# Kernel tuning notes

Measured on AMD Instinct MI355X. Metric: run time of the kernel, lower is better.

## Reference

```python
import jax, jax.numpy as jnp
import numpy as np

D_MODEL, D_STATE, D_CONV, D_INNER, DT_RANK = 96, 16, 3, 192, 6
BATCH, H, W = 4, 64, 64


def setup_inputs() -> dict:
    key = jax.random.key(0)
    ks = jax.random.split(key, 8)
    s = 0.02
    return {
        "x": jax.random.normal(ks[0], (BATCH, H, W, D_MODEL), jnp.float32),
        "in_proj_w": jax.random.normal(ks[1], (2 * D_INNER, D_MODEL), jnp.float32) * s,
        "conv_w": jax.random.normal(ks[2], (D_INNER, 1, D_CONV, D_CONV), jnp.float32) * s,
        "conv_b": jnp.zeros((D_INNER,), jnp.float32),
        "x_proj_w": jax.random.normal(ks[3], (4, DT_RANK + 2 * D_STATE, D_INNER), jnp.float32) * s,
        "dt_w": jax.random.normal(ks[4], (4, D_INNER, DT_RANK), jnp.float32) * s,
        # dt bias ~ inverse-softplus of dt in [1e-3, 1e-1] (roughly log-uniform negative values)
        "dt_b": jax.random.uniform(ks[5], (4, D_INNER), jnp.float32, minval=-6.0, maxval=-2.3),
        "A_logs": jnp.log(jnp.tile(jnp.arange(1, D_STATE + 1, dtype=jnp.float32), (4 * D_INNER, 1))),
        "Ds": jnp.ones((4 * D_INNER,), jnp.float32),
        "ln_w": jnp.ones((D_INNER,), jnp.float32),
        "ln_b": jnp.zeros((D_INNER,), jnp.float32),
        "out_proj_w": jax.random.normal(ks[6], (D_MODEL, D_INNER), jnp.float32) * s,
    }


def _ss2d(x, in_proj_w, conv_w, conv_b, x_proj_w, dt_w, dt_b, A_logs, Ds, ln_w, ln_b, out_proj_w):
    B, Hh, Ww, C = x.shape
    D = conv_w.shape[0]          # d_inner
    N = A_logs.shape[1]          # d_state
    R = dt_w.shape[2]            # dt_rank
    L = Hh * Ww
    K = 4

    xz = x @ in_proj_w.T                          # (B,H,W,2D)
    xi, z = jnp.split(xz, 2, axis=-1)
    xc = jnp.transpose(xi, (0, 3, 1, 2))          # (B,D,H,W)
    pad = (D_CONV - 1) // 2
    xc = jax.lax.conv_general_dilated(xc, conv_w, (1, 1), ((pad, pad), (pad, pad)),
                                      feature_group_count=D)
    xc = jax.nn.silu(xc + conv_b[None, :, None, None])

    # 4 scan directions: row-major, col-major, and their reverses
    x_flat = xc.reshape(B, D, L)
    x_tr = jnp.transpose(xc, (0, 1, 3, 2)).reshape(B, D, L)
    x_hwwh = jnp.stack([x_flat, x_tr], axis=1)                     # (B,2,D,L)
    xs = jnp.concatenate([x_hwwh, jnp.flip(x_hwwh, axis=-1)], axis=1)  # (B,K,D,L)

    x_dbl = jnp.einsum('bkdl,kcd->bkcl', xs, x_proj_w)
    dts, Bs, Cs = jnp.split(x_dbl, [R, R + N], axis=2)             # (B,K,R,L),(B,K,N,L),(B,K,N,L)
    dts = jnp.einsum('bkrl,kdr->bkdl', dts, dt_w)
    delta = jax.nn.softplus(dts + dt_b[None, :, :, None])          # (B,K,D,L)
    A = -jnp.exp(A_logs).reshape(K, D, N)                          # (K,D,N)

    # sequential selective scan over L (L-first for lax.scan)
    u_seq = jnp.moveaxis(xs, -1, 0)        # (L,B,K,D)
    dt_seq = jnp.moveaxis(delta, -1, 0)    # (L,B,K,D)
    B_seq = jnp.moveaxis(Bs, -1, 0)        # (L,B,K,N)
    C_seq = jnp.moveaxis(Cs, -1, 0)        # (L,B,K,N)

    def step(h, inp):
        u_t, dt_t, B_t, C_t = inp
        h = jnp.exp(dt_t[..., None] * A) * h + (dt_t * u_t)[..., None] * B_t[:, :, None, :]
        y = jnp.einsum('bkdn,bkn->bkd', h, C_t)
        return h, y

    h0 = jnp.zeros((B, K, D, N), jnp.float32)
    _, ys = jax.lax.scan(step, h0, (u_seq, dt_seq, B_seq, C_seq))
    out_y = jnp.moveaxis(ys, 0, -1) + Ds.reshape(K, D)[None, :, :, None] * xs  # (B,K,D,L)

    y1 = out_y[:, 0]
    y2 = jnp.transpose(out_y[:, 1].reshape(B, D, Ww, Hh), (0, 1, 3, 2)).reshape(B, D, L)
    y3 = jnp.flip(out_y[:, 2], axis=-1)
    y4 = jnp.transpose(jnp.flip(out_y[:, 3], axis=-1).reshape(B, D, Ww, Hh), (0, 1, 3, 2)).reshape(B, D, L)
    y = y1 + y2 + y3 + y4                                           # (B,D,L)

    y = jnp.transpose(y, (0, 2, 1)).reshape(B, Hh, Ww, D)
    mu = y.mean(-1, keepdims=True)
    var = y.var(-1, keepdims=True)
    y = (y - mu) * jax.lax.rsqrt(var + 1e-5) * ln_w + ln_b
    y = y * jax.nn.silu(z)
    return y @ out_proj_w.T


def reference(x, in_proj_w, conv_w, conv_b, x_proj_w, dt_w, dt_b, A_logs, Ds, ln_w, ln_b, out_proj_w):
    return _ss2d(x, in_proj_w, conv_w, conv_b, x_proj_w, dt_w, dt_b, A_logs, Ds, ln_w, ln_b, out_proj_w)
```

## Files before the change

kernel.cpp:

```cpp
#include <hip/hip_runtime.h>

constexpr int BATCH = 4;
constexpr int HS    = 64;
constexpr int WSZ   = 64;
constexpr int LSEQ  = 4096;
constexpr int DM    = 96;
constexpr int DI    = 192;
constexpr int NS    = 16;
constexpr int RK    = 6;
constexpr int KD    = 4;
constexpr int NCH   = 128;
constexpr int CLEN  = 32;
constexpr int XDS   = 160;
constexpr int GCH   = 16;
constexpr int GLEN  = NCH / GCH;

__device__ __forceinline__ int pos_of(int k, int l) {
  switch (k & 3) {
    case 0: return l;
    case 1: return ((l & 63) << 6) | (l >> 6);
    case 2: return LSEQ - 1 - l;
    default: { int lp = LSEQ - 1 - l; return ((lp & 63) << 6) | (lp >> 6); }
  }
}

__device__ __forceinline__ float softplus_f(float s) {
  return (s > 20.f) ? s : __logf(1.f + __expf(s));
}

__device__ __forceinline__ void pw16(float e, float* p) {
  float e2 = e * e, e4 = e2 * e2, e8 = e4 * e4;
  p[1] = e;       p[2] = e2;      p[3] = e2 * e;  p[4] = e4;
  p[5] = e4 * e;  p[6] = e4 * e2; p[7] = p[6] * e; p[8] = e8;
  p[9] = e8 * e;  p[10] = e8 * e2; p[11] = p[10] * e; p[12] = e8 * e4;
  p[13] = p[12] * e; p[14] = p[12] * e2; p[15] = p[14] * e; p[16] = e8 * e8;
}

__device__ __forceinline__ bool geo_check(const float* Al) {
  const float lntab[16] = {0.f, 0.6931472f, 1.0986123f, 1.3862944f, 1.6094379f,
                           1.7917595f, 1.9459101f, 2.0794415f, 2.1972246f, 2.3025851f,
                           2.3978953f, 2.4849066f, 2.5649494f, 2.6390573f, 2.7080502f,
                           2.7725887f};
  bool g = true;
  #pragma unroll
  for (int n = 0; n < NS; ++n)
    g = g && (fabsf(Al[n] - Al[0] - lntab[n]) <= 2e-3f);
  return g;
}

__device__ __forceinline__ float dt6(const float* w, float bsv, float4 t0, float4 t1) {
  return bsv + w[0]*t0.x + w[1]*t0.y + w[2]*t0.z + w[3]*t0.w + w[4]*t1.x + w[5]*t1.y;
}

__launch_bounds__(256)
__global__ void prep_weights(const float* __restrict__ xw, const float* __restrict__ ipw,
                             const float* __restrict__ opw, float* __restrict__ WcatT,
                             float* __restrict__ inpT, float* __restrict__ outpT) {
  int idx = blockIdx.x * 256 + threadIdx.x;
  if (idx < DI * XDS) {
    int col = idx / XDS, j = idx % XDS;
    int k = j / 40, jj = j % 40;
    float v = 0.f;
    int src = -1;
    if (jj < 16)      src = k * 38 + 6 + jj;
    else if (jj < 32) src = k * 38 + 22 + (jj - 16);
    else if (jj < 38) src = k * 38 + (jj - 32);
    if (src >= 0) v = xw[(size_t)src * DI + col];
    WcatT[idx] = v;
    return;
  }
  idx -= DI * XDS;
  if (idx < 2 * DI * DM) {
    int r = idx / DM, c = idx % DM;
    inpT[(size_t)c * (2 * DI) + r] = ipw[idx];
    return;
  }
  idx -= 2 * DI * DM;
  if (idx < DM * DI) {
    int r = idx / DI, c = idx % DI;
    outpT[(size_t)c * DM + r] = opw[idx];
  }
}

template <int NN, int KK, int TM, int KT>
__launch_bounds__(256)
__global__ void gemm_nt(const float* __restrict__ A, const float* __restrict__ BT,
                        float* __restrict__ C, int M) {
  constexpr int TN  = 64;
  constexpr int RPT = TM / 16;
  constexpr int SA  = KT + 4;
  constexpr int KQ  = KT / 4;
  __shared__ float As[TM][SA];
  __shared__ float Bs[KT][TN];
  const int t = threadIdx.x;
  const int row0 = blockIdx.y * TM;
  const int col0 = blockIdx.x * TN;
  const int tc = t & 15;
  const int tr = t >> 4;

  float acc[RPT][4];
  #pragma unroll
  for (int i = 0; i < RPT; ++i)
    { acc[i][0]=0.f; acc[i][1]=0.f; acc[i][2]=0.f; acc[i][3]=0.f; }

  for (int k0 = 0; k0 < KK; k0 += KT) {
    #pragma unroll 1
    for (int idx = t; idx < TM * KQ; idx += 256) {
      int r = idx / KQ, kq = idx % KQ;
      *(float4*)&As[r][kq * 4] =
          *(const float4*)&A[(size_t)(row0 + r) * KK + k0 + kq * 4];
    }
    #pragma unroll 1
    for (int idx = t; idx < KT * 16; idx += 256) {
      int kk = idx >> 4, cq = idx & 15;
      int col = col0 + cq * 4;
      float4 v = make_float4(0.f, 0.f, 0.f, 0.f);
      if (col < NN) v = *(const float4*)&BT[(size_t)(k0 + kk) * NN + col];
      *(float4*)&Bs[kk][cq * 4] = v;
    }
    __syncthreads();
    #pragma unroll 4
    for (int kk = 0; kk < KT; ++kk) {
      float4 bv = *(const float4*)&Bs[kk][tc * 4];
      #pragma unroll
      for (int i = 0; i < RPT; ++i) {
        float a = As[tr * RPT + i][kk];
        acc[i][0] += a * bv.x; acc[i][1] += a * bv.y;
        acc[i][2] += a * bv.z; acc[i][3] += a * bv.w;
      }
    }
    __syncthreads();
  }
  int c = col0 + tc * 4;
  if (c < NN) {
    #pragma unroll
    for (int i = 0; i < RPT; ++i) {
      size_t r0 = (size_t)(row0 + tr * RPT + i) * NN + c;
      *(float4*)&C[r0] = make_float4(acc[i][0], acc[i][1], acc[i][2], acc[i][3]);
    }
  }
}

__launch_bounds__(256)
__global__ void conv_silu(const float* __restrict__ xz, const float* __restrict__ cw,
                          const float* __restrict__ cb, float* __restrict__ xc) {
  int idx = blockIdx.x * 256 + threadIdx.x;
  int d = idx % DI;
  int p = (idx / DI) % LSEQ;
  int b = idx / (DI * LSEQ);
  int h = p >> 6, w = p & 63;
  float acc = cb[d];
  #pragma unroll
  for (int kh = 0; kh < 3; ++kh) {
    int hh = h + kh - 1;
    if ((unsigned)hh >= (unsigned)HS) continue;
    #pragma unroll
    for (int kw = 0; kw < 3; ++kw) {
      int ww = w + kw - 1;
      if ((unsigned)ww >= (unsigned)WSZ) continue;
      acc += xz[((size_t)b * LSEQ + (hh << 6) + ww) * (2 * DI) + d] * cw[d * 9 + kh * 3 + kw];
    }
  }
  xc[idx] = acc / (1.f + __expf(-acc));
}

__launch_bounds__(192)
__global__ void scan_phase1(const float* __restrict__ xc, const float* __restrict__ xdbl,
                            const float* __restrict__ Alog, const float* __restrict__ dtw,
                            const float* __restrict__ dtb,
                            float* __restrict__ hN, float* __restrict__ sumdB,
                            float* __restrict__ ypl) {
  const int d = threadIdx.x;
  const int ch = blockIdx.x, k = blockIdx.y, b = blockIdx.z;
  const int bk = b * KD + k;
  __shared__ float4 Bsh[CLEN * 10];
  #pragma unroll 1
  for (int idx = d; idx < CLEN * 10; idx += 192) {
    int j = idx / 10, q = idx % 10;
    int p = pos_of(k, ch * CLEN + j);
    Bsh[idx] = *(const float4*)&xdbl[(size_t)(b * LSEQ + p) * XDS + k * 40 + q * 4];
  }
  float Al[NS];
  {
    const float4* Ap = (const float4*)&Alog[((size_t)k * DI + d) * NS];
    #pragma unroll
    for (int q = 0; q < 4; ++q) {
      float4 a = Ap[q];
      Al[q*4+0] = a.x; Al[q*4+1] = a.y; Al[q*4+2] = a.z; Al[q*4+3] = a.w;
    }
  }
  const bool geo = geo_check(Al);
  const float An0 = -__expf(Al[0]);
  float w[RK];
  #pragma unroll
  for (int r = 0; r < RK; ++r) w[r] = dtw[((size_t)k * DI + d) * RK + r];
  const float bsv = dtb[k * DI + d];
  __syncthreads();

  float h[NS];
  #pragma unroll
  for (int n = 0; n < NS; ++n) h[n] = 0.f;
  float sumd = 0.f;
  float* yout = ypl + (size_t)bk * LSEQ * DI;
  const int l0 = ch * CLEN;
  if (geo) {
    #pragma unroll 2
    for (int j = 0; j < CLEN; ++j) {
      const int p = pos_of(k, l0 + j);
      const size_t bp = (size_t)b * LSEQ + p;
      float4 t0 = Bsh[j * 10 + 8], t1 = Bsh[j * 10 + 9];
      float dl = softplus_f(dt6(w, bsv, t0, t1));
      float du = dl * xc[bp * DI + d];
      float pw[17];
      pw16(__expf(dl * An0), pw);
      float y = 0.f;
      #pragma unroll
      for (int q = 0; q < 4; ++q) {
        float4 v  = Bsh[j * 10 + q];
        float4 c4 = Bsh[j * 10 + 4 + q];
        h[q*4+0] = pw[q*4+1] * h[q*4+0] + du * v.x; y += h[q*4+0] * c4.x;
        h[q*4+1] = pw[q*4+2] * h[q*4+1] + du * v.y; y += h[q*4+1] * c4.y;
        h[q*4+2] = pw[q*4+3] * h[q*4+2] + du * v.z; y += h[q*4+2] * c4.z;
        h[q*4+3] = pw[q*4+4] * h[q*4+3] + du * v.w; y += h[q*4+3] * c4.w;
      }
      sumd += dl;
      yout[(size_t)p * DI + d] = y;
    }
  } else {
    float An[NS];
    #pragma unroll
    for (int n = 0; n < NS; ++n) An[n] = -__expf(Al[n]);
    #pragma unroll 1
    for (int j = 0; j < CLEN; ++j) {
      const int p = pos_of(k, l0 + j);
      const size_t bp = (size_t)b * LSEQ + p;
      float4 t0 = Bsh[j * 10 + 8], t1 = Bsh[j * 10 + 9];
      float dl = softplus_f(dt6(w, bsv, t0, t1));
      float du = dl * xc[bp * DI + d];
      float y = 0.f;
      #pragma unroll
      for (int q = 0; q < 4; ++q) {
        float4 v  = Bsh[j * 10 + q];
        float4 c4 = Bsh[j * 10 + 4 + q];
        h[q*4+0] = __expf(dl * An[q*4+0]) * h[q*4+0] + du * v.x; y += h[q*4+0] * c4.x;
        h[q*4+1] = __expf(dl * An[q*4+1]) * h[q*4+1] + du * v.y; y += h[q*4+1] * c4.y;
        h[q*4+2] = __expf(dl * An[q*4+2]) * h[q*4+2] + du * v.z; y += h[q*4+2] * c4.z;
        h[q*4+3] = __expf(dl * An[q*4+3]) * h[q*4+3] + du * v.w; y += h[q*4+3] * c4.w;
      }
      sumd += dl;
      yout[(size_t)p * DI + d] = y;
    }
  }
  const size_t o = ((size_t)bk * NCH + ch) * DI + d;
  float4* Hp = (float4*)&hN[o * NS];
  #pragma unroll
  for (int q = 0; q < 4; ++q)
    Hp[q] = make_float4(h[q*4+0], h[q*4+1], h[q*4+2], h[q*4+3]);
  sumdB[o] = sumd;
}

__launch_bounds__(256)
__global__ void combine_a(const float* __restrict__ hN, const float* __restrict__ sumdB,
                          const float* __restrict__ Alog,
                          float* __restrict__ Wg, float* __restrict__ Tg) {
  const int tid = blockIdx.x * 256 + threadIdx.x;
  const int n  = tid & 15;
  int rem = tid >> 4;
  const int d  = rem % DI;  rem /= DI;
  const int g  = rem % GCH;
  const int bk = rem / GCH;
  const int k  = bk & 3;
  const float An = -__expf(Alog[((size_t)k * DI + d) * NS + n]);
  float W = 1.f, T = 0.f;
  #pragma unroll
  for (int j = 0; j < GLEN; ++j) {
    const int c = g * GLEN + j;
    const size_t o = ((size_t)bk * NCH + c) * DI + d;
    float w = __expf(An * sumdB[o]);
    T = hN[o * NS + n] + w * T;
    W *= w;
  }
  Wg[tid] = W;
  Tg[tid] = T;
}

__launch_bounds__(256)
__global__ void combine_b(const float* __restrict__ Wg, const float* __restrict__ Tg,
                          float* __restrict__ Hg) {
  const int tid = blockIdx.x * 256 + threadIdx.x;
  const int dn = tid & (DI * NS - 1);
  const int bk = tid / (DI * NS);
  float H = 0.f;
  #pragma unroll
  for (int g = 0; g < GCH; ++g) {
    const size_t o = ((size_t)(bk * GCH + g)) * (DI * NS) + dn;
    Hg[o] = H;
    H = Tg[o] + Wg[o] * H;
  }
}

__launch_bounds__(256)
__global__ void combine_c(float* __restrict__ hN, const float* __restrict__ sumdB,
                          const float* __restrict__ Alog, const float* __restrict__ Hg) {
  const int tid = blockIdx.x * 256 + threadIdx.x;
  const int n  = tid & 15;
  int rem = tid >> 4;
  const int d  = rem % DI;  rem /= DI;
  const int g  = rem % GCH;
  const int bk = rem / GCH;
  const int k  = bk & 3;
  const float An = -__expf(Alog[((size_t)k * DI + d) * NS + n]);
  float e = Hg[tid];
  #pragma unroll
  for (int j = 0; j < GLEN; ++j) {
    const int c = g * GLEN + j;
    const size_t o = ((size_t)bk * NCH + c) * DI + d;
    float w = __expf(An * sumdB[o]);
    float tmp = hN[o * NS + n];
    hN[o * NS + n] = e;
    e = tmp + w * e;
  }
}

__launch_bounds__(192)
__global__ void scan_corr(const float* __restrict__ xdbl, const float* __restrict__ Alog,
                          const float* __restrict__ dtw, const float* __restrict__ dtb,
                          const float* __restrict__ hin, float* __restrict__ ypl) {
  const int d = threadIdx.x;
  const int ch = blockIdx.x + 1;
  const int k = blockIdx.y, b = blockIdx.z;
  const int bk = b * KD + k;
  __shared__ float4 Bsh[CLEN * 6];
  {
    int idx = d;
    int j = idx / 6, q = idx % 6;
    int p = pos_of(k, ch * CLEN + j);
    Bsh[idx] = *(const float4*)&xdbl[(size_t)(b * LSEQ + p) * XDS + k * 40 + (q + 4) * 4];
  }
  float Al[NS];
  {
    const float4* Ap = (const float4*)&Alog[((size_t)k * DI + d) * NS];
    #pragma unroll
    for (int q = 0; q < 4; ++q) {
      float4 a = Ap[q];
      Al[q*4+0] = a.x; Al[q*4+1] = a.y; Al[q*4+2] = a.z; Al[q*4+3] = a.w;
    }
  }
  const bool geo = geo_check(Al);
  const float An0 = -__expf(Al[0]);
  float w[RK];
  #pragma unroll
  for (int r = 0; r < RK; ++r) w[r] = dtw[((size_t)k * DI + d) * RK + r];
  const float bsv = dtb[k * DI + d];

  float g[NS];
  {
    const size_t o = ((size_t)bk * NCH + ch) * DI + d;
    const float4* Hp = (const float4*)&hin[o * NS];
    #pragma unroll
    for (int q = 0; q < 4; ++q) {
      float4 v = Hp[q];
      g[q*4+0] = v.x; g[q*4+1] = v.y; g[q*4+2] = v.z; g[q*4+3] = v.w;
    }
  }
  __syncthreads();
  float* yout = ypl + (size_t)bk * LSEQ * DI;
  const int l0 = ch * CLEN;
  float cum = 0.f;
  if (geo) {
    #pragma unroll 2
    for (int j = 0; j < CLEN; ++j) {
      const int p = pos_of(k, l0 + j);
      float4 t0 = Bsh[j * 6 + 4], t1 = Bsh[j * 6 + 5];
      cum += softplus_f(dt6(w, bsv, t0, t1));
      float pw[17];
      pw16(__expf(cum * An0), pw);
      float y = 0.f;
      #pragma unroll
      for (int q = 0; q < 4; ++q) {
        float4 c4 = Bsh[j * 6 + q];
        y += (pw[q*4+1] * g[q*4+0]) * c4.x;
        y += (pw[q*4+2] * g[q*4+1]) * c4.y;
        y += (pw[q*4+3] * g[q*4+2]) * c4.z;
        y += (pw[q*4+4] * g[q*4+3]) * c4.w;
      }
      yout[(size_t)p * DI + d] += y;
    }
  } else {
    float An[NS];
    #pragma unroll
    for (int n = 0; n < NS; ++n) An[n] = -__expf(Al[n]);
    #pragma unroll 1
    for (int j = 0; j < CLEN; ++j) {
      const int p = pos_of(k, l0 + j);
      float4 t0 = Bsh[j * 6 + 4], t1 = Bsh[j * 6 + 5];
      cum += softplus_f(dt6(w, bsv, t0, t1));
      float y = 0.f;
      #pragma unroll
      for (int q = 0; q < 4; ++q) {
        float4 c4 = Bsh[j * 6 + q];
        y += (__expf(An[q*4+0] * cum) * g[q*4+0]) * c4.x;
        y += (__expf(An[q*4+1] * cum) * g[q*4+1]) * c4.y;
        y += (__expf(An[q*4+2] * cum) * g[q*4+2]) * c4.z;
        y += (__expf(An[q*4+3] * cum) * g[q*4+3]) * c4.w;
      }
      yout[(size_t)p * DI + d] += y;
    }
  }
}

__launch_bounds__(192)
__global__ void fuse_ln(const float* __restrict__ ypl, const float* __restrict__ xc,
                        const float* __restrict__ Ds, const float* __restrict__ xz,
                        const float* __restrict__ lnw, const float* __restrict__ lnb,
                        float* __restrict__ ymul) {
  const int row = blockIdx.x;
  const int b = row >> 12;
  const size_t pd = (size_t)row * DI + threadIdx.x;
  const int d = threadIdx.x;
  constexpr size_t PL = (size_t)LSEQ * DI;
  float u = xc[pd];
  float sDs = Ds[d] + Ds[DI + d] + Ds[2 * DI + d] + Ds[3 * DI + d];
  const size_t base = (size_t)(b * KD) * PL + pd - (size_t)b * PL;
  float y = ypl[base] + ypl[base + PL] + ypl[base + 2 * PL] + ypl[base + 3 * PL] + sDs * u;
  float s1 = y, s2 = y * y;
  #pragma unroll
  for (int off = 32; off; off >>= 1) {
    s1 += __shfl_xor(s1, off);
    s2 += __shfl_xor(s2, off);
  }
  __shared__ float r1[3], r2[3];
  int wid = d >> 6;
  if ((d & 63) == 0) { r1[wid] = s1; r2[wid] = s2; }
  __syncthreads();
  float S1 = r1[0] + r1[1] + r1[2];
  float S2 = r2[0] + r2[1] + r2[2];
  float mu = S1 * (1.f / DI);
  float var = S2 * (1.f / DI) - mu * mu;
  float yn = (y - mu) * rsqrtf(var + 1e-5f) * lnw[d] + lnb[d];
  float zv = xz[(size_t)row * (2 * DI) + DI + d];
  float g = zv / (1.f + __expf(-zv));
  ymul[pd] = yn * g;
}

extern "C" void kernel_launch(void* const* d_in, const int* in_sizes, int n_in,
                              void* d_out, int out_size, void* d_ws, size_t ws_size,
                              hipStream_t stream) {
  (void)in_sizes; (void)n_in; (void)out_size; (void)ws_size;
  const float* x          = (const float*)d_in[0];
  const float* in_proj_w  = (const float*)d_in[1];
  const float* conv_w     = (const float*)d_in[2];
  const float* conv_b     = (const float*)d_in[3];
  const float* x_proj_w   = (const float*)d_in[4];
  const float* dt_w       = (const float*)d_in[5];
  const float* dt_b       = (const float*)d_in[6];
  const float* A_logs     = (const float*)d_in[7];
  const float* Ds         = (const float*)d_in[8];
  const float* ln_w       = (const float*)d_in[9];
  const float* ln_b       = (const float*)d_in[10];
  const float* out_proj_w = (const float*)d_in[11];
  float* out = (float*)d_out;
  float* ws  = (float*)d_ws;

  constexpr size_t SZ_XZ    = (size_t)BATCH * LSEQ * 2 * DI;
  constexpr size_t SZ_XC    = (size_t)BATCH * LSEQ * DI;
  constexpr size_t SZ_XD    = (size_t)BATCH * LSEQ * XDS;
  constexpr size_t SZ_HN    = (size_t)BATCH * KD * NCH * DI * NS;
  constexpr size_t SZ_SUMD  = (size_t)BATCH * KD * NCH * DI;
  constexpr size_t SZ_YPL   = (size_t)BATCH * KD * LSEQ * DI;
  constexpr size_t SZ_G     = (size_t)BATCH * KD * GCH * DI * NS;

  float* xz    = ws;
  float* xc    = xz + SZ_XZ;
  float* xdbl  = xc + SZ_XC;
  float* hN    = xdbl + SZ_XD;
  float* sumd  = hN + SZ_HN;
  float* ypl   = sumd + SZ_SUMD;
  float* WcatT = ypl + SZ_YPL;
  float* inpT  = WcatT + (size_t)DI * XDS;
  float* outpT = inpT + (size_t)DM * 2 * DI;
  float* Wg    = outpT + (size_t)DI * DM;
  float* Tg    = Wg + SZ_G;
  float* Hg    = Tg + SZ_G;
  float* ymul  = hN;

  const int M = BATCH * LSEQ;
  const int SG = BATCH * KD * GCH * DI * NS;
  const int PREP = DI * XDS + 2 * DI * DM + DM * DI;

  prep_weights<<<(PREP + 255) / 256, 256, 0, stream>>>(x_proj_w, in_proj_w, out_proj_w,
                                                       WcatT, inpT, outpT);
  gemm_nt<2 * DI, DM, 64, 96><<<dim3(6, M / 64), 256, 0, stream>>>(x, inpT, xz, M);
  conv_silu<<<(BATCH * LSEQ * DI) / 256, 256, 0, stream>>>(xz, conv_w, conv_b, xc);
  gemm_nt<XDS, DI, 64, 96><<<dim3(3, M / 64), 256, 0, stream>>>(xc, WcatT, xdbl, M);
  scan_phase1<<<dim3(NCH, KD, BATCH), 192, 0, stream>>>(xc, xdbl, A_logs, dt_w, dt_b,
                                                        hN, sumd, ypl);
  combine_a<<<SG / 256, 256, 0, stream>>>(hN, sumd, A_logs, Wg, Tg);
  combine_b<<<(BATCH * KD * DI * NS) / 256, 256, 0, stream>>>(Wg, Tg, Hg);
  combine_c<<<SG / 256, 256, 0, stream>>>(hN, sumd, A_logs, Hg);
  scan_corr<<<dim3(NCH - 1, KD, BATCH), 192, 0, stream>>>(xdbl, A_logs, dt_w, dt_b,
                                                          hN, ypl);
  fuse_ln<<<M, DI, 0, stream>>>(ypl, xc, Ds, xz, ln_w, ln_b, ymul);
  gemm_nt<DM, DI, 64, 96><<<dim3(2, M / 64), 256, 0, stream>>>(ymul, outpT, out, M);
}
```

Before: 213.2 us.

## Split SSM state dimension across thread pairs in scan kernels

Both chunked scan kernels now use two threads per channel, each holding half of the 16 state entries. A lane-xor shuffle sums the partial outputs and only the even lane stores. The goal is more threads per block and fewer registers per thread, which shortens each thread's serial recurrence and raises occupancy. The cost is duplicated dt/softplus/exp work in both lanes, an extra shuffle each step, and half-idle lanes on the output stores.

```diff
diff --git a/kernel.cpp b/kernel.cpp
--- a/kernel.cpp
+++ b/kernel.cpp
@@ -28,12 +28,11 @@
   return (s > 20.f) ? s : __logf(1.f + __expf(s));
 }
 
-__device__ __forceinline__ void pw16(float e, float* p) {
-  float e2 = e * e, e4 = e2 * e2, e8 = e4 * e4;
-  p[1] = e;       p[2] = e2;      p[3] = e2 * e;  p[4] = e4;
-  p[5] = e4 * e;  p[6] = e4 * e2; p[7] = p[6] * e; p[8] = e8;
-  p[9] = e8 * e;  p[10] = e8 * e2; p[11] = p[10] * e; p[12] = e8 * e4;
-  p[13] = p[12] * e; p[14] = p[12] * e2; p[15] = p[14] * e; p[16] = e8 * e8;
+__device__ __forceinline__ void pw8h(float e, float base, float* p) {
+  float e2 = e * e, e4 = e2 * e2;
+  float e3 = e2 * e, e5 = e4 * e, e6 = e4 * e2, e7 = e6 * e, e8 = e4 * e4;
+  p[0] = base * e;  p[1] = base * e2; p[2] = base * e3; p[3] = base * e4;
+  p[4] = base * e5; p[5] = base * e6; p[6] = base * e7; p[7] = base * e8;
 }
 
 __device__ __forceinline__ bool geo_check(const float* Al) {
@@ -164,21 +163,21 @@
   xc[idx] = acc / (1.f + __expf(-acc));
 }
 
-__launch_bounds__(192)
+__launch_bounds__(384)
 __global__ void scan_phase1(const float* __restrict__ xc, const float* __restrict__ xdbl,
                             const float* __restrict__ Alog, const float* __restrict__ dtw,
                             const float* __restrict__ dtb,
                             float* __restrict__ hN, float* __restrict__ sumdB,
                             float* __restrict__ ypl) {
-  const int d = threadIdx.x;
+  const int t = threadIdx.x;
+  const int d = t >> 1, half = t & 1;
   const int ch = blockIdx.x, k = blockIdx.y, b = blockIdx.z;
   const int bk = b * KD + k;
   __shared__ float4 Bsh[CLEN * 10];
-  #pragma unroll 1
-  for (int idx = d; idx < CLEN * 10; idx += 192) {
-    int j = idx / 10, q = idx % 10;
+  if (t < CLEN * 10) {
+    int j = t / 10, q = t % 10;
     int p = pos_of(k, ch * CLEN + j);
-    Bsh[idx] = *(const float4*)&xdbl[(size_t)(b * LSEQ + p) * XDS + k * 40 + q * 4];
+    Bsh[t] = *(const float4*)&xdbl[(size_t)(b * LSEQ + p) * XDS + k * 40 + q * 4];
   }
   float Al[NS];
   {
@@ -197,12 +196,13 @@
   const float bsv = dtb[k * DI + d];
   __syncthreads();
 
-  float h[NS];
-  #pragma unroll
-  for (int n = 0; n < NS; ++n) h[n] = 0.f;
+  float h[8];
+  #pragma unroll
+  for (int n = 0; n < 8; ++n) h[n] = 0.f;
   float sumd = 0.f;
   float* yout = ypl + (size_t)bk * LSEQ * DI;
   const int l0 = ch * CLEN;
+  const int hb = half * 2;
   if (geo) {
     #pragma unroll 2
     for (int j = 0; j < CLEN; ++j) {
@@ -211,25 +211,30 @@
       float4 t0 = Bsh[j * 10 + 8], t1 = Bsh[j * 10 + 9];
       float dl = softplus_f(dt6(w, bsv, t0, t1));
       float du = dl * xc[bp * DI + d];
-      float pw[17];
-      pw16(__expf(dl * An0), pw);
+      float e = __expf(dl * An0);
+      float e2 = e * e, e4 = e2 * e2, e8 = e4 * e4;
+      float base = half ? e8 : 1.f;
+      float pw[8];
+      pw8h(e, base, pw);
+      float4 v0 = Bsh[j * 10 + hb],     v1 = Bsh[j * 10 + hb + 1];
+      float4 c0 = Bsh[j * 10 + 4 + hb], c1 = Bsh[j * 10 + 4 + hb + 1];
       float y = 0.f;
-      #pragma unroll
-      for (int q = 0; q < 4; ++q) {
-        float4 v  = Bsh[j * 10 + q];
-        float4 c4 = Bsh[j * 10 + 4 + q];
-        h[q*4+0] = pw[q*4+1] * h[q*4+0] + du * v.x; y += h[q*4+0] * c4.x;
-        h[q*4+1] = pw[q*4+2] * h[q*4+1] + du * v.y; y += h[q*4+1] * c4.y;
-        h[q*4+2] = pw[q*4+3] * h[q*4+2] + du * v.z; y += h[q*4+2] * c4.z;
-        h[q*4+3] = pw[q*4+4] * h[q*4+3] + du * v.w; y += h[q*4+3] * c4.w;
-      }
+      h[0] = pw[0] * h[0] + du * v0.x; y += h[0] * c0.x;
+      h[1] = pw[1] * h[1] + du * v0.y; y += h[1] * c0.y;
+      h[2] = pw[2] * h[2] + du * v0.z; y += h[2] * c0.z;
+      h[3] = pw[3] * h[3] + du * v0.w; y += h[3] * c0.w;
+      h[4] = pw[4] * h[4] + du * v1.x; y += h[4] * c1.x;
+      h[5] = pw[5] * h[5] + du * v1.y; y += h[5] * c1.y;
+      h[6] = pw[6] * h[6] + du * v1.z; y += h[6] * c1.z;
+      h[7] = pw[7] * h[7] + du * v1.w; y += h[7] * c1.w;
+      y += __shfl_xor(y, 1);
       sumd += dl;
-      yout[(size_t)p * DI + d] = y;
+      if (!half) yout[(size_t)p * DI + d] = y;
     }
   } else {
-    float An[NS];
+    float An[8];
     #pragma unroll
-    for (int n = 0; n < NS; ++n) An[n] = -__expf(Al[n]);
+    for (int n = 0; n < 8; ++n) An[n] = -__expf(Al[half * 8 + n]);
     #pragma unroll 1
     for (int j = 0; j < CLEN; ++j) {
       const int p = pos_of(k, l0 + j);
@@ -237,26 +242,27 @@
       float4 t0 = Bsh[j * 10 + 8], t1 = Bsh[j * 10 + 9];
       float dl = softplus_f(dt6(w, bsv, t0, t1));
       float du = dl * xc[bp * DI + d];
+      float4 v0 = Bsh[j * 10 + hb],     v1 = Bsh[j * 10 + hb + 1];
+      float4 c0 = Bsh[j * 10 + 4 + hb], c1 = Bsh[j * 10 + 4 + hb + 1];
       float y = 0.f;
-      #pragma unroll
-      for (int q = 0; q < 4; ++q) {
-        float4 v  = Bsh[j * 10 + q];
-        float4 c4 = Bsh[j * 10 + 4 + q];
-        h[q*4+0] = __expf(dl * An[q*4+0]) * h[q*4+0] + du * v.x; y += h[q*4+0] * c4.x;
-        h[q*4+1] = __expf(dl * An[q*4+1]) * h[q*4+1] + du * v.y; y += h[q*4+1] * c4.y;
-        h[q*4+2] = __expf(dl * An[q*4+2]) * h[q*4+2] + du * v.z; y += h[q*4+2] * c4.z;
-        h[q*4+3] = __expf(dl * An[q*4+3]) * h[q*4+3] + du * v.w; y += h[q*4+3] * c4.w;
-      }
+      h[0] = __expf(dl*An[0]) * h[0] + du * v0.x; y += h[0] * c0.x;
+      h[1] = __expf(dl*An[1]) * h[1] + du * v0.y; y += h[1] * c0.y;
+      h[2] = __expf(dl*An[2]) * h[2] + du * v0.z; y += h[2] * c0.z;
+      h[3] = __expf(dl*An[3]) * h[3] + du * v0.w; y += h[3] * c0.w;
+      h[4] = __expf(dl*An[4]) * h[4] + du * v1.x; y += h[4] * c1.x;
+      h[5] = __expf(dl*An[5]) * h[5] + du * v1.y; y += h[5] * c1.y;
+      h[6] = __expf(dl*An[6]) * h[6] + du * v1.z; y += h[6] * c1.z;
+      h[7] = __expf(dl*An[7]) * h[7] + du * v1.w; y += h[7] * c1.w;
+      y += __shfl_xor(y, 1);
       sumd += dl;
-      yout[(size_t)p * DI + d] = y;
+      if (!half) yout[(size_t)p * DI + d] = y;
     }
   }
   const size_t o = ((size_t)bk * NCH + ch) * DI + d;
   float4* Hp = (float4*)&hN[o * NS];
-  #pragma unroll
-  for (int q = 0; q < 4; ++q)
-    Hp[q] = make_float4(h[q*4+0], h[q*4+1], h[q*4+2], h[q*4+3]);
-  sumdB[o] = sumd;
+  Hp[half * 2 + 0] = make_float4(h[0], h[1], h[2], h[3]);
+  Hp[half * 2 + 1] = make_float4(h[4], h[5], h[6], h[7]);
+  if (!half) sumdB[o] = sumd;
 }
 
 __launch_bounds__(256)
@@ -322,20 +328,20 @@
   }
 }
 
-__launch_bounds__(192)
+__launch_bounds__(384)
 __global__ void scan_corr(const float* __restrict__ xdbl, const float* __restrict__ Alog,
                           const float* __restrict__ dtw, const float* __restrict__ dtb,
                           const float* __restrict__ hin, float* __restrict__ ypl) {
-  const int d = threadIdx.x;
+  const int t = threadIdx.x;
+  const int d = t >> 1, half = t & 1;
   const int ch = blockIdx.x + 1;
   const int k = blockIdx.y, b = blockIdx.z;
   const int bk = b * KD + k;
   __shared__ float4 Bsh[CLEN * 6];
-  {
-    int idx = d;
-    int j = idx / 6, q = idx % 6;
+  if (t < CLEN * 6) {
+    int j = t / 6, q = t % 6;
     int p = pos_of(k, ch * CLEN + j);
-    Bsh[idx] = *(const float4*)&xdbl[(size_t)(b * LSEQ + p) * XDS + k * 40 + (q + 4) * 4];
+    Bsh[t] = *(const float4*)&xdbl[(size_t)(b * LSEQ + p) * XDS + k * 40 + (q + 4) * 4];
   }
   float Al[NS];
   {
@@ -353,19 +359,19 @@
   for (int r = 0; r < RK; ++r) w[r] = dtw[((size_t)k * DI + d) * RK + r];
   const float bsv = dtb[k * DI + d];
 
-  float g[NS];
+  float g[8];
   {
     const size_t o = ((size_t)bk * NCH + ch) * DI + d;
     const float4* Hp = (const float4*)&hin[o * NS];
-    #pragma unroll
-    for (int q = 0; q < 4; ++q) {
-      float4 v = Hp[q];
-      g[q*4+0] = v.x; g[q*4+1] = v.y; g[q*4+2] = v.z; g[q*4+3] = v.w;
-    }
+    float4 v = Hp[half * 2 + 0];
+    g[0]=v.x; g[1]=v.y; g[2]=v.z; g[3]=v.w;
+    float4 u = Hp[half * 2 + 1];
+    g[4]=u.x; g[5]=u.y; g[6]=u.z; g[7]=u.w;
   }
   __syncthreads();
   float* yout = ypl + (size_t)bk * LSEQ * DI;
   const int l0 = ch * CLEN;
+  const int hb = half * 2;
   float cum = 0.f;
   if (geo) {
     #pragma unroll 2
@@ -373,38 +379,41 @@
       const int p = pos_of(k, l0 + j);
       float4 t0 = Bsh[j * 6 + 4], t1 = Bsh[j * 6 + 5];
       cum += softplus_f(dt6(w, bsv, t0, t1));
-      float pw[17];
-      pw16(__expf(cum * An0), pw);
+      float e = __expf(cum * An0);
+      float e2 = e * e, e4 = e2 * e2, e8 = e4 * e4;
+      float base = half ? e8 : 1.f;
+      float pw[8];
+      pw8h(e, base, pw);
+      float4 c0 = Bsh[j * 6 + hb], c1 = Bsh[j * 6 + hb + 1];
       float y = 0.f;
-      #pragma unroll
-      for (int q = 0; q < 4; ++q) {
-        float4 c4 = Bsh[j * 6 + q];
-        y += (pw[q*4+1] * g[q*4+0]) * c4.x;
-        y += (pw[q*4+2] * g[q*4+1]) * c4.y;
-        y += (pw[q*4+3] * g[q*4+2]) * c4.z;
-        y += (pw[q*4+4] * g[q*4+3]) * c4.w;
-      }
-      yout[(size_t)p * DI + d] += y;
+      y += (pw[0] * g[0]) * c0.x; y += (pw[1] * g[1]) * c0.y;
+      y += (pw[2] * g[2]) * c0.z; y += (pw[3] * g[3]) * c0.w;
+      y += (pw[4] * g[4]) * c1.x; y += (pw[5] * g[5]) * c1.y;
+      y += (pw[6] * g[6]) * c1.z; y += (pw[7] * g[7]) * c1.w;
+      y += __shfl_xor(y, 1);
+      if (!half) yout[(size_t)p * DI + d] += y;
     }
   } else {
-    float An[NS];
+    float An[8];
     #pragma unroll
-    for (int n = 0; n < NS; ++n) An[n] = -__expf(Al[n]);
+    for (int n = 0; n < 8; ++n) An[n] = -__expf(Al[half * 8 + n]);
     #pragma unroll 1
     for (int j = 0; j < CLEN; ++j) {
       const int p = pos_of(k, l0 + j);
       float4 t0 = Bsh[j * 6 + 4], t1 = Bsh[j * 6 + 5];
       cum += softplus_f(dt6(w, bsv, t0, t1));
+      float4 c0 = Bsh[j * 6 + hb], c1 = Bsh[j * 6 + hb + 1];
       float y = 0.f;
-      #pragma unroll
-      for (int q = 0; q < 4; ++q) {
-        float4 c4 = Bsh[j * 6 + q];
-        y += (__expf(An[q*4+0] * cum) * g[q*4+0]) * c4.x;
-        y += (__expf(An[q*4+1] * cum) * g[q*4+1]) * c4.y;
-        y += (__expf(An[q*4+2] * cum) * g[q*4+2]) * c4.z;
-        y += (__expf(An[q*4+3] * cum) * g[q*4+3]) * c4.w;
-      }
-      yout[(size_t)p * DI + d] += y;
+      y += (__expf(An[0] * cum) * g[0]) * c0.x;
+      y += (__expf(An[1] * cum) * g[1]) * c0.y;
+      y += (__expf(An[2] * cum) * g[2]) * c0.z;
+      y += (__expf(An[3] * cum) * g[3]) * c0.w;
+      y += (__expf(An[4] * cum) * g[4]) * c1.x;
+      y += (__expf(An[5] * cum) * g[5]) * c1.y;
+      y += (__expf(An[6] * cum) * g[6]) * c1.z;
+      y += (__expf(An[7] * cum) * g[7]) * c1.w;
+      y += __shfl_xor(y, 1);
+      if (!half) yout[(size_t)p * DI + d] += y;
     }
   }
 }
@@ -493,12 +502,12 @@
   gemm_nt<2 * DI, DM, 64, 96><<<dim3(6, M / 64), 256, 0, stream>>>(x, inpT, xz, M);
   conv_silu<<<(BATCH * LSEQ * DI) / 256, 256, 0, stream>>>(xz, conv_w, conv_b, xc);
   gemm_nt<XDS, DI, 64, 96><<<dim3(3, M / 64), 256, 0, stream>>>(xc, WcatT, xdbl, M);
-  scan_phase1<<<dim3(NCH, KD, BATCH), 192, 0, stream>>>(xc, xdbl, A_logs, dt_w, dt_b,
+  scan_phase1<<<dim3(NCH, KD, BATCH), 384, 0, stream>>>(xc, xdbl, A_logs, dt_w, dt_b,
                                                         hN, sumd, ypl);
   combine_a<<<SG / 256, 256, 0, stream>>>(hN, sumd, A_logs, Wg, Tg);
   combine_b<<<(BATCH * KD * DI * NS) / 256, 256, 0, stream>>>(Wg, Tg, Hg);
   combine_c<<<SG / 256, 256, 0, stream>>>(hN, sumd, A_logs, Hg);
-  scan_corr<<<dim3(NCH - 1, KD, BATCH), 192, 0, stream>>>(xdbl, A_logs, dt_w, dt_b,
+  scan_corr<<<dim3(NCH - 1, KD, BATCH), 384, 0, stream>>>(xdbl, A_logs, dt_w, dt_b,
                                                           hN, ypl);
   fuse_ln<<<M, DI, 0, stream>>>(ypl, xc, Ds, xz, ln_w, ln_b, ymul);
   gemm_nt<DM, DI, 64, 96><<<dim3(2, M / 64), 256, 0, stream>>>(ymul, outpT, out, M);
```

New measurement: 243.1 us. +14.0%, slower.

## Fuse chunk-combine kernels into one block-local scan; split scan blocks by channel

Applied to the files above, without the earlier changes.

Replaces the three combine kernels (combine_a, combine_b, combine_c) with a single combine_all kernel. Each block handles one (b,k,d) and does the group-level carry scan in shared memory, holding the decay factors and chunk states in registers, so the Wg/Tg/Hg global round trips and two launches go away. scan_phase1 and scan_corr now launch 64-thread blocks over a three-way channel split, giving more, smaller blocks for occupancy. In exchange, each of those blocks reloads the shared B/C chunk data that the three channel groups used to share.

```diff
diff --git a/kernel.cpp b/kernel.cpp
--- a/kernel.cpp
+++ b/kernel.cpp
@@ -164,18 +164,20 @@
   xc[idx] = acc / (1.f + __expf(-acc));
 }
 
-__launch_bounds__(192)
+__launch_bounds__(64)
 __global__ void scan_phase1(const float* __restrict__ xc, const float* __restrict__ xdbl,
                             const float* __restrict__ Alog, const float* __restrict__ dtw,
                             const float* __restrict__ dtb,
                             float* __restrict__ hN, float* __restrict__ sumdB,
                             float* __restrict__ ypl) {
-  const int d = threadIdx.x;
-  const int ch = blockIdx.x, k = blockIdx.y, b = blockIdx.z;
+  const int t = threadIdx.x;
+  const int ch = blockIdx.x, b = blockIdx.z;
+  const int k = blockIdx.y / 3;
+  const int d = (blockIdx.y % 3) * 64 + t;
   const int bk = b * KD + k;
   __shared__ float4 Bsh[CLEN * 10];
   #pragma unroll 1
-  for (int idx = d; idx < CLEN * 10; idx += 192) {
+  for (int idx = t; idx < CLEN * 10; idx += 64) {
     int j = idx / 10, q = idx % 10;
     int p = pos_of(k, ch * CLEN + j);
     Bsh[idx] = *(const float4*)&xdbl[(size_t)(b * LSEQ + p) * XDS + k * 40 + q * 4];
@@ -260,79 +262,64 @@
 }
 
 __launch_bounds__(256)
-__global__ void combine_a(const float* __restrict__ hN, const float* __restrict__ sumdB,
-                          const float* __restrict__ Alog,
-                          float* __restrict__ Wg, float* __restrict__ Tg) {
-  const int tid = blockIdx.x * 256 + threadIdx.x;
-  const int n  = tid & 15;
-  int rem = tid >> 4;
-  const int d  = rem % DI;  rem /= DI;
-  const int g  = rem % GCH;
-  const int bk = rem / GCH;
-  const int k  = bk & 3;
+__global__ void combine_all(float* __restrict__ hN, const float* __restrict__ sumdB,
+                            const float* __restrict__ Alog) {
+  const int t = threadIdx.x;
+  const int n = t & 15;
+  const int g = t >> 4;
+  const int d = blockIdx.x;
+  const int k = blockIdx.y, b = blockIdx.z;
+  const int bk = b * KD + k;
   const float An = -__expf(Alog[((size_t)k * DI + d) * NS + n]);
+  __shared__ float Wl[GCH][NS], Tl[GCH][NS], Hl[GCH][NS];
+
+  float wreg[GLEN], hreg[GLEN];
   float W = 1.f, T = 0.f;
   #pragma unroll
   for (int j = 0; j < GLEN; ++j) {
     const int c = g * GLEN + j;
     const size_t o = ((size_t)bk * NCH + c) * DI + d;
-    float w = __expf(An * sumdB[o]);
-    T = hN[o * NS + n] + w * T;
-    W *= w;
-  }
-  Wg[tid] = W;
-  Tg[tid] = T;
-}
-
-__launch_bounds__(256)
-__global__ void combine_b(const float* __restrict__ Wg, const float* __restrict__ Tg,
-                          float* __restrict__ Hg) {
-  const int tid = blockIdx.x * 256 + threadIdx.x;
-  const int dn = tid & (DI * NS - 1);
-  const int bk = tid / (DI * NS);
-  float H = 0.f;
-  #pragma unroll
-  for (int g = 0; g < GCH; ++g) {
-    const size_t o = ((size_t)(bk * GCH + g)) * (DI * NS) + dn;
-    Hg[o] = H;
-    H = Tg[o] + Wg[o] * H;
-  }
-}
-
-__launch_bounds__(256)
-__global__ void combine_c(float* __restrict__ hN, const float* __restrict__ sumdB,
-                          const float* __restrict__ Alog, const float* __restrict__ Hg) {
-  const int tid = blockIdx.x * 256 + threadIdx.x;
-  const int n  = tid & 15;
-  int rem = tid >> 4;
-  const int d  = rem % DI;  rem /= DI;
-  const int g  = rem % GCH;
-  const int bk = rem / GCH;
-  const int k  = bk & 3;
-  const float An = -__expf(Alog[((size_t)k * DI + d) * NS + n]);
-  float e = Hg[tid];
+    float wv = __expf(An * sumdB[o]);
+    float hv = hN[o * NS + n];
+    wreg[j] = wv; hreg[j] = hv;
+    T = hv + wv * T;
+    W *= wv;
+  }
+  Wl[g][n] = W; Tl[g][n] = T;
+  __syncthreads();
+  if (g == 0) {
+    float H = 0.f;
+    #pragma unroll
+    for (int g2 = 0; g2 < GCH; ++g2) {
+      float Wv = Wl[g2][n], Tv = Tl[g2][n];
+      Hl[g2][n] = H;
+      H = Tv + Wv * H;
+    }
+  }
+  __syncthreads();
+  float e = Hl[g][n];
   #pragma unroll
   for (int j = 0; j < GLEN; ++j) {
     const int c = g * GLEN + j;
     const size_t o = ((size_t)bk * NCH + c) * DI + d;
-    float w = __expf(An * sumdB[o]);
-    float tmp = hN[o * NS + n];
     hN[o * NS + n] = e;
-    e = tmp + w * e;
-  }
-}
-
-__launch_bounds__(192)
+    e = hreg[j] + wreg[j] * e;
+  }
+}
+
+__launch_bounds__(64)
 __global__ void scan_corr(const float* __restrict__ xdbl, const float* __restrict__ Alog,
                           const float* __restrict__ dtw, const float* __restrict__ dtb,
                           const float* __restrict__ hin, float* __restrict__ ypl) {
-  const int d = threadIdx.x;
+  const int t = threadIdx.x;
   const int ch = blockIdx.x + 1;
-  const int k = blockIdx.y, b = blockIdx.z;
+  const int b = blockIdx.z;
+  const int k = blockIdx.y / 3;
+  const int d = (blockIdx.y % 3) * 64 + t;
   const int bk = b * KD + k;
   __shared__ float4 Bsh[CLEN * 6];
-  {
-    int idx = d;
+  #pragma unroll 1
+  for (int idx = t; idx < CLEN * 6; idx += 64) {
     int j = idx / 6, q = idx % 6;
     int p = pos_of(k, ch * CLEN + j);
     Bsh[idx] = *(const float4*)&xdbl[(size_t)(b * LSEQ + p) * XDS + k * 40 + (q + 4) * 4];
@@ -468,7 +455,6 @@
   constexpr size_t SZ_HN    = (size_t)BATCH * KD * NCH * DI * NS;
   constexpr size_t SZ_SUMD  = (size_t)BATCH * KD * NCH * DI;
   constexpr size_t SZ_YPL   = (size_t)BATCH * KD * LSEQ * DI;
-  constexpr size_t SZ_G     = (size_t)BATCH * KD * GCH * DI * NS;
 
   float* xz    = ws;
   float* xc    = xz + SZ_XZ;
@@ -479,13 +465,9 @@
   float* WcatT = ypl + SZ_YPL;
   float* inpT  = WcatT + (size_t)DI * XDS;
   float* outpT = inpT + (size_t)DM * 2 * DI;
-  float* Wg    = outpT + (size_t)DI * DM;
-  float* Tg    = Wg + SZ_G;
-  float* Hg    = Tg + SZ_G;
   float* ymul  = hN;
 
   const int M = BATCH * LSEQ;
-  const int SG = BATCH * KD * GCH * DI * NS;
   const int PREP = DI * XDS + 2 * DI * DM + DM * DI;
 
   prep_weights<<<(PREP + 255) / 256, 256, 0, stream>>>(x_proj_w, in_proj_w, out_proj_w,
@@ -493,13 +475,11 @@
   gemm_nt<2 * DI, DM, 64, 96><<<dim3(6, M / 64), 256, 0, stream>>>(x, inpT, xz, M);
   conv_silu<<<(BATCH * LSEQ * DI) / 256, 256, 0, stream>>>(xz, conv_w, conv_b, xc);
   gemm_nt<XDS, DI, 64, 96><<<dim3(3, M / 64), 256, 0, stream>>>(xc, WcatT, xdbl, M);
-  scan_phase1<<<dim3(NCH, KD, BATCH), 192, 0, stream>>>(xc, xdbl, A_logs, dt_w, dt_b,
-                                                        hN, sumd, ypl);
-  combine_a<<<SG / 256, 256, 0, stream>>>(hN, sumd, A_logs, Wg, Tg);
-  combine_b<<<(BATCH * KD * DI * NS) / 256, 256, 0, stream>>>(Wg, Tg, Hg);
-  combine_c<<<SG / 256, 256, 0, stream>>>(hN, sumd, A_logs, Hg);
-  scan_corr<<<dim3(NCH - 1, KD, BATCH), 192, 0, stream>>>(xdbl, A_logs, dt_w, dt_b,
-                                                          hN, ypl);
+  scan_phase1<<<dim3(NCH, KD * 3, BATCH), 64, 0, stream>>>(xc, xdbl, A_logs, dt_w, dt_b,
+                                                           hN, sumd, ypl);
+  combine_all<<<dim3(DI, KD, BATCH), 256, 0, stream>>>(hN, sumd, A_logs);
+  scan_corr<<<dim3(NCH - 1, KD * 3, BATCH), 64, 0, stream>>>(xdbl, A_logs, dt_w, dt_b,
+                                                             hN, ypl);
   fuse_ln<<<M, DI, 0, stream>>>(ypl, xc, Ds, xz, ln_w, ln_b, ymul);
   gemm_nt<DM, DI, 64, 96><<<dim3(2, M / 64), 256, 0, stream>>>(ymul, outpT, out, M);
 }
```

Result: slower. 218.5 us (+2.5%).
